# Performance work log

Measured on AMD Instinct MI355X. Metric: run time of the kernel, lower is better.

Reference implementation:

```python
import jax, jax.numpy as jnp
import numpy as np

B, C_IN, H, W = 8, 1024, 18, 80
FEAT = 1024
A = 32      # anchors per location
NCLS = 3    # classes
NREG = 13
K = 3       # kernel size
K2 = K * K
EPS = 1e-5  # BatchNorm eps


def conv2d(x, w, b):
    y = jax.lax.conv_general_dilated(x, w, (1, 1), ((1, 1), (1, 1)),
                                     dimension_numbers=('NCHW', 'OIHW', 'NCHW'))
    return y + b[None, :, None, None]


def bn_eval(x, g, b):
    # eval-mode BatchNorm2d with running_mean=0, running_var=1
    return x * (g / jnp.sqrt(1.0 + EPS))[None, :, None, None] + b[None, :, None, None]


def anchor_flatten(x, d):
    # [B, A*d, H, W] -> permute(0,2,3,1) -> [B, H*W*A, d]
    Bx, Cx, Hx, Wx = x.shape
    return jnp.transpose(x, (0, 2, 3, 1)).reshape(Bx, Hx * Wx * (Cx // d), d)


def bilinear_gather(x, py, px):
    # x: [B,C,H,W]; py/px: [B,K2,H,W] float coords -> [B,C,K2,H,W], zero outside
    Bx, Cx, Hx, Wx = x.shape
    y0 = jnp.floor(py); x0 = jnp.floor(px)
    wy1 = py - y0; wx1 = px - x0
    wy0 = 1.0 - wy1; wx0 = 1.0 - wx1
    xf = x.reshape(Bx, Cx, Hx * Wx)

    def g(yy, xx):
        valid = ((yy >= 0) & (yy < Hx) & (xx >= 0) & (xx < Wx)).astype(x.dtype)
        yc = jnp.clip(yy, 0, Hx - 1).astype(jnp.int32)
        xc = jnp.clip(xx, 0, Wx - 1).astype(jnp.int32)
        idx = (yc * Wx + xc).reshape(Bx, -1)
        vals = jax.vmap(lambda xi, ii: xi[:, ii])(xf, idx).reshape(Bx, Cx, K2, Hx, Wx)
        return vals * valid[:, None]

    return (g(y0, x0) * (wy0 * wx0)[:, None] + g(y0, x0 + 1) * (wy0 * wx1)[:, None]
            + g(y0 + 1, x0) * (wy1 * wx0)[:, None] + g(y0 + 1, x0 + 1) * (wy1 * wx1)[:, None])


def mdcn(x, off_w, off_b, w, b):
    # ModulatedDeformConvPack (DCNv2): 3x3 conv -> (dy, dx, mask), then modulated deform conv
    out = conv2d(x, off_w, off_b)                        # [B, 3*K2, H, W]
    dy, dx, m = out[:, :K2], out[:, K2:2 * K2], jax.nn.sigmoid(out[:, 2 * K2:])
    ky, kx = jnp.meshgrid(jnp.arange(K, dtype=x.dtype), jnp.arange(K, dtype=x.dtype), indexing='ij')
    base_y = jnp.arange(x.shape[2], dtype=x.dtype)[None, None, :, None] - 1.0 + ky.reshape(1, K2, 1, 1)
    base_x = jnp.arange(x.shape[3], dtype=x.dtype)[None, None, None, :] - 1.0 + kx.reshape(1, K2, 1, 1)
    sampled = bilinear_gather(x, base_y + dy, base_x + dx) * m[:, None]   # [B,C,K2,H,W]
    O = w.shape[0]
    return jnp.einsum('bckhw,ock->bohw', sampled, w.reshape(O, w.shape[1], K2)) + b[None, :, None, None]


def setup_inputs() -> dict:
    key = jax.random.key(0)
    ks = jax.random.split(key, 10)
    s1 = 1.0 / np.sqrt(C_IN * K2)
    s2 = 1.0 / np.sqrt(FEAT * K2)
    rn = lambda k, sh, sc: jax.random.normal(k, sh, jnp.float32) * sc
    return {
        'features': jax.random.normal(ks[0], (B, C_IN, H, W), jnp.float32),
        'cls_w1': rn(ks[1], (FEAT, C_IN, K, K), s1), 'cls_b1': jnp.zeros((FEAT,), jnp.float32),
        'cls_w2': rn(ks[2], (FEAT, FEAT, K, K), s2), 'cls_b2': jnp.zeros((FEAT,), jnp.float32),
        'cls_w3': rn(ks[3], (A * NCLS, FEAT, K, K), s2), 'cls_b3': jnp.zeros((A * NCLS,), jnp.float32),
        'off_w': rn(ks[4], (3 * K2, C_IN, K, K), s1), 'off_b': jnp.zeros((3 * K2,), jnp.float32),
        'dcn_w': rn(ks[5], (FEAT, C_IN, K, K), s1), 'dcn_b': jnp.zeros((FEAT,), jnp.float32),
        'bn1_g': jnp.ones((FEAT,), jnp.float32), 'bn1_b': jnp.zeros((FEAT,), jnp.float32),
        'reg_w2': rn(ks[6], (FEAT, FEAT, K, K), s2), 'reg_b2': jnp.zeros((FEAT,), jnp.float32),
        'bn2_g': jnp.ones((FEAT,), jnp.float32), 'bn2_b': jnp.zeros((FEAT,), jnp.float32),
        'reg_w3': rn(ks[7], (A * NREG, FEAT, K, K), s2), 'reg_b3': jnp.zeros((A * NREG,), jnp.float32),
    }


def reference(features, cls_w1, cls_b1, cls_w2, cls_b2, cls_w3, cls_b3,
              off_w, off_b, dcn_w, dcn_b, bn1_g, bn1_b,
              reg_w2, reg_b2, bn2_g, bn2_b, reg_w3, reg_b3):
    # cls branch (Dropout2d is identity in eval)
    h = jax.nn.relu(conv2d(features, cls_w1, cls_b1))
    h = jax.nn.relu(conv2d(h, cls_w2, cls_b2))
    cls_preds = anchor_flatten(conv2d(h, cls_w3, cls_b3), NCLS)   # [B, H*W*A, NCLS]
    # reg branch: modulated deformable conv -> BN -> ReLU -> conv -> BN -> ReLU -> conv
    r = jax.nn.relu(bn_eval(mdcn(features, off_w, off_b, dcn_w, dcn_b), bn1_g, bn1_b))
    r = jax.nn.relu(bn_eval(conv2d(r, reg_w2, reg_b2), bn2_g, bn2_b))
    reg_preds = anchor_flatten(conv2d(r, reg_w3, reg_b3), NREG)   # [B, H*W*A, NREG]
    return (cls_preds, reg_preds)
```

## Files before the change

kernel.cpp:

```cpp
#include <hip/hip_runtime.h>
#include <math.h>

typedef short short8 __attribute__((ext_vector_type(8)));
typedef float f32x4 __attribute__((ext_vector_type(4)));
typedef unsigned short u16;
typedef unsigned int u32;

#define GAS(p) ((__attribute__((address_space(1))) void*)(p))
#define LAS(p) ((__attribute__((address_space(3))) void*)(p))

namespace {

constexpr int HW   = 1440;
constexpr int PBAT = 20 * 82 * 1024;

__device__ __forceinline__ u16 f2bf(float f) {
  u32 u = __float_as_uint(f);
  return (u16)((u + 0x7FFFu + ((u >> 16) & 1u)) >> 16);
}
__device__ __forceinline__ float bf2f(u16 h) {
  return __uint_as_float(((u32)h) << 16);
}

__global__ __launch_bounds__(256)
void transpose_feat(const float* __restrict__ src, u16* __restrict__ dst) {
  __shared__ float tile[128][17];
  const int bh = blockIdx.y;
  const int b = bh / 18, h = bh % 18;
  const int wt = blockIdx.x % 5, ct = blockIdx.x / 5;
  const int w0 = wt * 16, c0 = ct * 128;
  const int tid = threadIdx.x;
#pragma unroll
  for (int it = 0; it < 8; ++it) {
    int idx = it * 256 + tid;
    int c = idx >> 4, w = idx & 15;
    tile[c][w] = src[((size_t)(b * 1024 + c0 + c) * 18 + h) * 80 + w0 + w];
  }
  __syncthreads();
  const int px = tid >> 4, cq = tid & 15;
  union { uint4 u; u16 s[8]; } pk;
#pragma unroll
  for (int j = 0; j < 8; ++j) pk.s[j] = f2bf(tile[cq * 8 + j][px]);
  *(uint4*)(dst + ((size_t)(b * 20 + h + 1) * 82 + (w0 + px + 1)) * 1024 + c0 + cq * 8) = pk.u;
}

struct RepackArgs {
  const float* src[7];
  u16* dst[7];
  int O[7];
  int start[7];
  int nseg;
};

__global__ __launch_bounds__(256)
void repack_all(RepackArgs ra) {
  int blk = blockIdx.x;
  int seg = 0;
#pragma unroll
  for (int i = 1; i < 7; ++i)
    if (i < ra.nseg && blk >= ra.start[i]) seg = i;
  const float* src = ra.src[seg];
  u16* dst = ra.dst[seg];
  const int O = ra.O[seg];
  int idx = (blk - ra.start[seg]) * 256 + threadIdx.x;
  if (idx >= O * 128) return;
  int o = idx >> 7, c8 = idx & 127;
  const float* s = src + (size_t)o * 9216 + (size_t)c8 * 72;
  float v[72];
#pragma unroll
  for (int i = 0; i < 18; ++i) {
    float4 f = *(const float4*)(s + i * 4);
    v[i * 4 + 0] = f.x; v[i * 4 + 1] = f.y; v[i * 4 + 2] = f.z; v[i * 4 + 3] = f.w;
  }
#pragma unroll
  for (int t = 0; t < 9; ++t) {
    union { uint4 u; u16 h[8]; } pk;
#pragma unroll
    for (int j = 0; j < 8; ++j) pk.h[j] = f2bf(v[j * 9 + t]);
    *(uint4*)(dst + ((size_t)t * O + o) * 1024 + c8 * 8) = pk.u;
  }
}

__device__ __forceinline__
void sample_body(int k, int lp, int pix0, int Npc,
                 const u16* __restrict__ featP, const float* __restrict__ offp,
                 u16* __restrict__ spl, int tid) {
  const int p = pix0 + lp;
  const int c8 = tid & 15;
  int b = p / HW, hw = p - b * HW;
  int h = hw / 80, w = hw - h * 80;
  float dy = offp[p * 27 + k];
  float dx = offp[p * 27 + 9 + k];
  float ml = offp[p * 27 + 18 + k];
  float m = 1.f / (1.f + expf(-ml));
  float py = (float)(h - 1 + k / 3) + dy;
  float px = (float)(w - 1 + (k % 3)) + dx;
  float y0f = floorf(py), x0f = floorf(px);
  float wy1 = py - y0f, wx1 = px - x0f;
  float wy0 = 1.f - wy1, wx0 = 1.f - wx1;
  int y0 = (int)y0f, x0 = (int)x0f;
  int ya = min(max(y0, -1), 18),  yb = min(max(y0 + 1, -1), 18);
  int xa = min(max(x0, -1), 80),  xb = min(max(x0 + 1, -1), 80);
  const u16* base = featP + (size_t)b * PBAT;
  const u16* r00 = base + ((size_t)(ya + 1) * 82 + (xa + 1)) * 1024;
  const u16* r01 = base + ((size_t)(ya + 1) * 82 + (xb + 1)) * 1024;
  const u16* r10 = base + ((size_t)(yb + 1) * 82 + (xa + 1)) * 1024;
  const u16* r11 = base + ((size_t)(yb + 1) * 82 + (xb + 1)) * 1024;
  float w00 = wy0 * wx0 * m, w01 = wy0 * wx1 * m;
  float w10 = wy1 * wx0 * m, w11 = wy1 * wx1 * m;
  u16* dst = spl + ((size_t)k * Npc + lp) * 1024;
  for (int c = c8 * 8; c < 1024; c += 128) {
    union { uint4 u; u16 h[8]; } a, bq, cq2, d, o;
    a.u   = *(const uint4*)(r00 + c);
    bq.u  = *(const uint4*)(r01 + c);
    cq2.u = *(const uint4*)(r10 + c);
    d.u   = *(const uint4*)(r11 + c);
#pragma unroll
    for (int j = 0; j < 8; ++j) {
      float v = w00 * bf2f(a.h[j]) + w01 * bf2f(bq.h[j]) +
                w10 * bf2f(cq2.h[j]) + w11 * bf2f(d.h[j]);
      o.h[j] = f2bf(v);
    }
    *(uint4*)(dst + c) = o.u;
  }
}

__global__ __launch_bounds__(256)
void sample_standalone(const u16* __restrict__ featP, const float* __restrict__ offp,
                       u16* __restrict__ spl, int pix0, int Npc) {
  sample_body(blockIdx.y, blockIdx.x * 16 + (threadIdx.x >> 4), pix0, Npc,
              featP, offp, spl, threadIdx.x);
}

struct Job {
  const u16* W; const u16* B;
  const float* bias; const float* bng; const float* bnb;
  void* out; int Co; int pix0; int Npc;
};

template<int FLAGS>
__device__ __forceinline__ void gemm_body(const Job J, int px, int oy) {
  constexpr bool PLANES  = (FLAGS & 1) != 0;
  constexpr bool F32OUT  = (FLAGS & 2) != 0;
  constexpr bool HASBN   = (FLAGS & 4) != 0;
  constexpr bool HASRELU = (FLAGS & 8) != 0;

  __shared__ __align__(16) u16 As[128 * 32];
  __shared__ __align__(16) u16 Bs[128 * 32];
  const int tid = threadIdx.x;
  const int wv = tid >> 6, lane = tid & 63;
  const int o0 = oy * 128;
  const int p0 = J.pix0 + px * 128;

  const int lr = lane >> 2;
  const int qs = (lane & 3) ^ ((lane >> 3) & 3);
  int aoff[2], boff[2];
#pragma unroll
  for (int s = 0; s < 2; ++s) {
    int r = (wv * 2 + s) * 16 + lr;
    int o = min(o0 + r, J.Co - 1);
    aoff[s] = o * 1024 + qs * 8;
    int p = p0 + r;
    if (PLANES) {
      boff[s] = (p - J.pix0) * 1024 + qs * 8;
    } else {
      int b = p / HW, hw = p - b * HW;
      int h = hw / 80, w = hw - h * 80;
      boff[s] = ((b * 20 + h) * 82 + w) * 1024 + qs * 8;
    }
  }
  u16* aDst = As + (wv * 2) * 512;
  u16* bDst = Bs + (wv * 2) * 512;

  const int wm = wv >> 1, wn = wv & 1;
  const int frm = lane & 15;
  const int kq = lane >> 4;
  const int sel = (kq ^ ((lane >> 1) & 3)) * 16;

  f32x4 acc[4][4];
#pragma unroll
  for (int i = 0; i < 4; ++i)
#pragma unroll
    for (int j = 0; j < 4; ++j) acc[i][j] = (f32x4)0.f;

  for (int t = 0; t < 9; ++t) {
    const u16* Wt = J.W + (size_t)t * J.Co * 1024;
    const u16* Bt = J.B + (PLANES ? (size_t)t * (size_t)J.Npc * 1024
                                  : (size_t)(((t / 3) * 82 + (t % 3)) * 1024));
    for (int cc = 0; cc < 1024; cc += 32) {
      __syncthreads();
#pragma unroll
      for (int s = 0; s < 2; ++s) {
        __builtin_amdgcn_global_load_lds(GAS(Wt + aoff[s] + cc), LAS(aDst + s * 512), 16, 0, 0);
        __builtin_amdgcn_global_load_lds(GAS(Bt + boff[s] + cc), LAS(bDst + s * 512), 16, 0, 0);
      }
      __syncthreads();
      uint4 af[4], bf4[4];
#pragma unroll
      for (int i = 0; i < 4; ++i) {
        af[i]  = *(const uint4*)((const char*)As + (wm * 64 + i * 16 + frm) * 64 + sel);
        bf4[i] = *(const uint4*)((const char*)Bs + (wn * 64 + i * 16 + frm) * 64 + sel);
      }
#pragma unroll
      for (int i = 0; i < 4; ++i) {
        short8 a = __builtin_bit_cast(short8, af[i]);
#pragma unroll
        for (int j = 0; j < 4; ++j) {
          short8 b = __builtin_bit_cast(short8, bf4[j]);
          acc[i][j] = __builtin_amdgcn_mfma_f32_16x16x32_bf16(a, b, acc[i][j], 0, 0, 0);
        }
      }
    }
  }

  size_t obase[4];
#pragma unroll
  for (int j = 0; j < 4; ++j) {
    int pn = p0 + wn * 64 + j * 16 + frm;
    if (F32OUT) {
      obase[j] = (size_t)pn * J.Co;
    } else {
      int b = pn / HW, hw = pn - b * HW;
      int h = hw / 80, w = hw - h * 80;
      obase[j] = ((size_t)(b * 20 + h + 1) * 82 + (w + 1)) * 1024;
    }
  }
#pragma unroll
  for (int i = 0; i < 4; ++i) {
    int o = o0 + wm * 64 + i * 16 + kq * 4;
    float bi[4], sc[4], sh[4];
#pragma unroll
    for (int r = 0; r < 4; ++r) {
      int oc = min(o + r, J.Co - 1);
      bi[r] = J.bias[oc];
      if (HASBN) { sc[r] = J.bng[oc] * rsqrtf(1.f + 1e-5f); sh[r] = J.bnb[oc]; }
    }
#pragma unroll
    for (int j = 0; j < 4; ++j) {
      float v[4];
#pragma unroll
      for (int r = 0; r < 4; ++r) {
        float x = acc[i][j][r] + bi[r];
        if (HASBN) x = x * sc[r] + sh[r];
        if (HASRELU) x = fmaxf(x, 0.f);
        v[r] = x;
      }
      if (F32OUT) {
        float* op = (float*)J.out;
#pragma unroll
        for (int r = 0; r < 4; ++r)
          if (o + r < J.Co) op[obase[j] + o + r] = v[r];
      } else {
        u16* op = (u16*)J.out;
        ushort4 pk;
        pk.x = f2bf(v[0]); pk.y = f2bf(v[1]); pk.z = f2bf(v[2]); pk.w = f2bf(v[3]);
        *(ushort4*)(op + obase[j] + o) = pk;
      }
    }
  }
}

template<int F0, int F1>
__global__ __launch_bounds__(256)
void gemm_dual(Job j0, Job j1, int ysplit) {
  int y = blockIdx.y;
  if (y < ysplit) gemm_body<F0>(j0, blockIdx.x, y);
  else            gemm_body<F1>(j1, blockIdx.x, y - ysplit);
}

template<int FLAGS>
__device__ __forceinline__ void gemm8_body(const Job J, char* ldsb, int px, int oy) {
  constexpr bool PLANES  = (FLAGS & 1) != 0;
  constexpr bool F32OUT  = (FLAGS & 2) != 0;
  constexpr bool HASBN   = (FLAGS & 4) != 0;
  constexpr bool HASRELU = (FLAGS & 8) != 0;

  const int tid = threadIdx.x;
  const int w = tid >> 6, lane = tid & 63;
  const int o0 = oy * 256;
  const int p0 = J.pix0 + px * 256;

  const int lr3 = lane >> 3;
  const int srcC = ((lane & 7) ^ lr3) << 3;
  u32 aEl[2][2], bEl[2][2];
#pragma unroll
  for (int h = 0; h < 2; ++h)
#pragma unroll
  for (int s = 0; s < 2; ++s) {
    int crow = (w * 2 + s) * 8 + lr3;
    int o = min(o0 + h * 128 + crow, J.Co - 1);
    aEl[h][s] = (u32)o * 1024u;
    int p = p0 + h * 128 + crow;
    if (PLANES) {
      bEl[h][s] = (u32)(p - J.pix0) * 1024u;
    } else {
      int b = p / HW, hw = p - b * HW;
      int hh = hw / 80, ww = hw - hh * 80;
      bEl[h][s] = (u32)((b * 20 + hh) * 82 + ww) * 1024u;
    }
  }

  auto STAGE_A = [&](int buf, int h, int kt) {
    int tap = kt >> 4, cc = (kt & 15) << 6;
    const u16* src = J.W + (size_t)tap * (size_t)J.Co * 1024 + cc + srcC;
    char* dst = ldsb + (buf * 65536 + h * 16384 + (w * 2) * 1024);
    __builtin_amdgcn_global_load_lds(GAS(src + aEl[h][0]), LAS(dst), 16, 0, 0);
    __builtin_amdgcn_global_load_lds(GAS(src + aEl[h][1]), LAS(dst + 1024), 16, 0, 0);
  };
  auto STAGE_B = [&](int buf, int h, int kt) {
    int tap = kt >> 4, cc = (kt & 15) << 6;
    size_t tb = PLANES ? (size_t)tap * (size_t)J.Npc * 1024
                       : (size_t)(((tap / 3) * 82 + (tap % 3)) * 1024);
    const u16* src = J.B + tb + cc + srcC;
    char* dst = ldsb + (buf * 65536 + 32768 + h * 16384 + (w * 2) * 1024);
    __builtin_amdgcn_global_load_lds(GAS(src + bEl[h][0]), LAS(dst), 16, 0, 0);
    __builtin_amdgcn_global_load_lds(GAS(src + bEl[h][1]), LAS(dst + 1024), 16, 0, 0);
  };

  const int wm2 = w >> 2, wn2 = w & 3;
  const int rA = wm2 * 64 + (lane & 15);
  const int rB = wn2 * 32 + (lane & 15);
  const int xsw = (lane & 7) << 4;
  const int csw0 = (((lane >> 4) << 4)) ^ xsw;
  const int csw1 = (64 | ((lane >> 4) << 4)) ^ xsw;

  f32x4 acc[4][4][2];
#pragma unroll
  for (int q = 0; q < 4; ++q)
#pragma unroll
  for (int m = 0; m < 4; ++m)
#pragma unroll
  for (int n = 0; n < 2; ++n) acc[q][m][n] = (f32x4)0.f;

  uint4 aF[4][2], bF[2][2];

#define G8_RD_A(BUF, AH)                                                      \
  { const char* Ab_ = ldsb + ((BUF) * 65536 + (AH) * 16384);                  \
    _Pragma("unroll") for (int m_ = 0; m_ < 4; ++m_) {                        \
      aF[m_][0] = *(const uint4*)(Ab_ + (rA + m_ * 16) * 128 + csw0);         \
      aF[m_][1] = *(const uint4*)(Ab_ + (rA + m_ * 16) * 128 + csw1); } }

#define G8_RD_B(BUF, BH)                                                      \
  { const char* Bb_ = ldsb + ((BUF) * 65536 + 32768 + (BH) * 16384);          \
    _Pragma("unroll") for (int n_ = 0; n_ < 2; ++n_) {                        \
      bF[n_][0] = *(const uint4*)(Bb_ + (rB + n_ * 16) * 128 + csw0);         \
      bF[n_][1] = *(const uint4*)(Bb_ + (rB + n_ * 16) * 128 + csw1); } }

#define G8_MMA(Q)                                                             \
    __builtin_amdgcn_s_barrier();                                             \
    asm volatile("s_waitcnt lgkmcnt(0)" ::: "memory");                        \
    __builtin_amdgcn_sched_barrier(0);                                        \
    __builtin_amdgcn_s_setprio(1);                                            \
    _Pragma("unroll") for (int m_ = 0; m_ < 4; ++m_)                          \
    _Pragma("unroll") for (int n_ = 0; n_ < 2; ++n_)                          \
    _Pragma("unroll") for (int k_ = 0; k_ < 2; ++k_)                          \
      acc[Q][m_][n_] = __builtin_amdgcn_mfma_f32_16x16x32_bf16(               \
          __builtin_bit_cast(short8, aF[m_][k_]),                             \
          __builtin_bit_cast(short8, bF[n_][k_]), acc[Q][m_][n_], 0, 0, 0);   \
    __builtin_amdgcn_s_setprio(0);

#define G8_VMW asm volatile("s_waitcnt vmcnt(4)" ::: "memory");
#define G8_BAR __builtin_amdgcn_s_barrier();

  STAGE_A(0, 0, 0); STAGE_A(0, 1, 0); STAGE_B(0, 0, 0); STAGE_B(0, 1, 0);
  STAGE_A(1, 0, 1); STAGE_B(1, 0, 1);
  G8_VMW
  __builtin_amdgcn_s_barrier();

  for (int it = 0; it < 72; ++it) {
    const int kt = it * 2;
    const int k2 = min(kt + 2, 143), k3 = min(kt + 3, 143);
    G8_RD_A(0, 0) G8_RD_B(0, 0) STAGE_B(1, 1, kt + 1); G8_MMA(0) G8_BAR
    G8_RD_B(0, 1)               STAGE_A(1, 1, kt + 1); G8_MMA(1) G8_BAR
    G8_RD_A(0, 1) G8_RD_B(0, 0) STAGE_A(0, 0, k2);     G8_MMA(2) G8_BAR
    G8_RD_B(0, 1)               STAGE_B(0, 0, k2);     G8_MMA(3) G8_VMW G8_BAR
    G8_RD_A(1, 0) G8_RD_B(1, 0) STAGE_B(0, 1, k2);     G8_MMA(0) G8_BAR
    G8_RD_B(1, 1)               STAGE_A(0, 1, k2);     G8_MMA(1) G8_BAR
    G8_RD_A(1, 1) G8_RD_B(1, 0) STAGE_A(1, 0, k3);     G8_MMA(2) G8_BAR
    G8_RD_B(1, 1)               STAGE_B(1, 0, k3);     G8_MMA(3) G8_VMW G8_BAR
  }

#undef G8_RD_A
#undef G8_RD_B
#undef G8_MMA
#undef G8_VMW
#undef G8_BAR

  const int kq = lane >> 4, fr = lane & 15;
  size_t pixB[2][2];
#pragma unroll
  for (int bh = 0; bh < 2; ++bh)
#pragma unroll
  for (int n = 0; n < 2; ++n) {
    int p = p0 + bh * 128 + wn2 * 32 + n * 16 + fr;
    if (F32OUT) {
      pixB[bh][n] = (size_t)p * J.Co;
    } else {
      int b = p / HW, hw = p - b * HW;
      int hh = hw / 80, ww = hw - hh * 80;
      pixB[bh][n] = ((size_t)(b * 20 + hh + 1) * 82 + (ww + 1)) * 1024;
    }
  }
#pragma unroll
  for (int ah = 0; ah < 2; ++ah)
#pragma unroll
  for (int m = 0; m < 4; ++m) {
    int ob = o0 + ah * 128 + wm2 * 64 + m * 16 + kq * 4;
    float bi[4], sc[4], sh[4];
#pragma unroll
    for (int r = 0; r < 4; ++r) {
      int oc = min(ob + r, J.Co - 1);
      bi[r] = J.bias[oc];
      if (HASBN) { sc[r] = J.bng[oc] * rsqrtf(1.f + 1e-5f); sh[r] = J.bnb[oc]; }
    }
#pragma unroll
    for (int bh = 0; bh < 2; ++bh)
#pragma unroll
    for (int n = 0; n < 2; ++n) {
      float v[4];
#pragma unroll
      for (int r = 0; r < 4; ++r) {
        float x = acc[ah * 2 + bh][m][n][r] + bi[r];
        if (HASBN) x = x * sc[r] + sh[r];
        if (HASRELU) x = fmaxf(x, 0.f);
        v[r] = x;
      }
      if (F32OUT) {
        float* op = (float*)J.out;
#pragma unroll
        for (int r = 0; r < 4; ++r)
          if (ob + r < J.Co) op[pixB[bh][n] + ob + r] = v[r];
      } else {
        u16* op = (u16*)J.out;
        ushort4 pk;
        pk.x = f2bf(v[0]); pk.y = f2bf(v[1]); pk.z = f2bf(v[2]); pk.w = f2bf(v[3]);
        *(ushort4*)(op + pixB[bh][n] + ob) = pk;
      }
    }
  }
}

template<int F0, int F1>
__global__ __launch_bounds__(512, 2)
void gemm8_dual(Job j0, Job j1, int n0, int mt0, int mt1) {
  __shared__ __align__(16) char ldsb[131072];
  int x = blockIdx.x;
  if (x < n0) gemm8_body<F0>(j0, ldsb, x / mt0, x % mt0);
  else { x -= n0; gemm8_body<F1>(j1, ldsb, x / mt1, x % mt1); }
}

template<int F0>
__global__ __launch_bounds__(512, 2)
void gemm8_sample(Job j, const u16* __restrict__ featP, const float* __restrict__ offp,
                  u16* __restrict__ spl, int n0, int mt0) {
  __shared__ __align__(16) char ldsb[131072];
  int x = blockIdx.x;
  if (x < n0) {
    gemm8_body<F0>(j, ldsb, x / mt0, x % mt0);
  } else {
    int sidx = x - n0;
    int k = sidx / 360, bs = sidx % 360;
    sample_body(k, bs * 32 + ((int)threadIdx.x >> 4), 0, 11520,
                featP, offp, spl, (int)threadIdx.x);
  }
}

}

extern "C" void kernel_launch(void* const* d_in, const int* in_sizes, int n_in,
                              void* d_out, int out_size, void* d_ws, size_t ws_size,
                              hipStream_t stream) {
  const float* feat   = (const float*)d_in[0];
  const float* cls_w1 = (const float*)d_in[1];
  const float* cls_b1 = (const float*)d_in[2];
  const float* cls_w2 = (const float*)d_in[3];
  const float* cls_b2 = (const float*)d_in[4];
  const float* cls_w3 = (const float*)d_in[5];
  const float* cls_b3 = (const float*)d_in[6];
  const float* off_w  = (const float*)d_in[7];
  const float* off_b  = (const float*)d_in[8];
  const float* dcn_w  = (const float*)d_in[9];
  const float* dcn_b  = (const float*)d_in[10];
  const float* bn1_g  = (const float*)d_in[11];
  const float* bn1_b  = (const float*)d_in[12];
  const float* reg_w2 = (const float*)d_in[13];
  const float* reg_b2 = (const float*)d_in[14];
  const float* bn2_g  = (const float*)d_in[15];
  const float* bn2_b  = (const float*)d_in[16];
  const float* reg_w3 = (const float*)d_in[17];
  const float* reg_b3 = (const float*)d_in[18];
  float* outp = (float*)d_out;

  const size_t ACTB = 26869760;
  char* wsb = (char*)d_ws;
  u16* featP = (u16*)(wsb);
  u16* bufA  = (u16*)(wsb + ACTB);
  u16* bufB  = (u16*)(wsb + 2 * ACTB);
  u16* wts   = (u16*)(wsb + 3 * ACTB);
  float* offp = (float*)(wsb + 3 * ACTB + 85432320);
  u16* spl   = (u16*)(wsb + 3 * ACTB + 85432320 + 1244160);
  const size_t BASE = 3 * ACTB + 85432320 + 1244160;
  const size_t SPLB = (size_t)9 * 11520 * 1024 * 2;

  u16* offT = wts;
  u16* w1T  = wts + 248832;
  u16* w2T  = wts + 9686016;
  u16* w3T  = wts + 19123200;
  u16* dcnT = wts + 20007936;
  u16* r2T  = wts + 29445120;
  u16* r3T  = wts + 38882304;

  dim3 blk(256);

  hipMemsetAsync(featP, 0, 3 * ACTB, stream);
  transpose_feat<<<dim3(40, 144), blk, 0, stream>>>(feat, featP);

  {
    RepackArgs ra;
    const float* s[7] = {off_w, cls_w1, cls_w2, cls_w3, dcn_w, reg_w2, reg_w3};
    u16* d[7] = {offT, w1T, w2T, w3T, dcnT, r2T, r3T};
    int  O[7] = {27, 1024, 1024, 96, 1024, 1024, 416};
    int acc = 0;
    for (int i = 0; i < 7; ++i) {
      ra.src[i] = s[i]; ra.dst[i] = d[i]; ra.O[i] = O[i]; ra.start[i] = acc;
      acc += (O[i] * 128 + 255) / 256;
    }
    ra.nseg = 7;
    repack_all<<<dim3(acc), blk, 0, stream>>>(ra);
  }

  Job jOff  = {offT, featP, off_b, nullptr, nullptr, offp, 27, 0, 0};
  Job jCls1 = {w1T, featP, cls_b1, nullptr, nullptr, bufA, 1024, 0, 0};
  Job jCls2 = {w2T, bufA, cls_b2, nullptr, nullptr, bufB, 1024, 0, 0};
  Job jCls3 = {w3T, bufB, cls_b3, nullptr, nullptr, outp, 96, 0, 0};
  Job jReg2 = {r2T, bufA, reg_b2, bn2_g, bn2_b, bufB, 1024, 0, 0};
  Job jReg3 = {r3T, bufB, reg_b3, nullptr, nullptr, outp + 1105920, 416, 0, 0};

  if (ws_size >= BASE + SPLB) {
    dim3 b512(512);
    gemm8_dual<8, 2><<<dim3(225), b512, 0, stream>>>(jCls1, jOff, 180, 4, 1);
    gemm8_sample<8><<<dim3(180 + 3240), b512, 0, stream>>>(jCls2, featP, offp, spl, 180, 4);
    Job jDcn = {dcnT, spl, dcn_b, bn1_g, bn1_b, bufA, 1024, 0, 11520};
    gemm8_dual<1 | 4 | 8, 2><<<dim3(225), b512, 0, stream>>>(jDcn, jCls3, 180, 4, 1);
    gemm8_dual<4 | 8, 4 | 8><<<dim3(180), b512, 0, stream>>>(jReg2, jReg2, 180, 4, 4);
    gemm_dual<2, 2><<<dim3(90, 4), blk, 0, stream>>>(jReg3, jReg3, 4);
  } else {
    gemm_dual<8, 2><<<dim3(90, 9), blk, 0, stream>>>(jCls1, jOff, 8);
    gemm_dual<8, 8><<<dim3(90, 8), blk, 0, stream>>>(jCls2, jCls2, 8);
    size_t avail = ws_size > BASE ? ws_size - BASE : 0;
    int tiles = (int)(avail / 2359296);
    if (tiles < 1) tiles = 1;
    if (tiles > 90) tiles = 90;
    for (int t0 = 0; t0 < 90; t0 += tiles) {
      int nt = (90 - t0) < tiles ? (90 - t0) : tiles;
      int pix0 = t0 * 128, np = nt * 128;
      sample_standalone<<<dim3(nt * 8, 9), blk, 0, stream>>>(featP, offp, spl, pix0, np);
      Job jDcn = {dcnT, spl, dcn_b, bn1_g, bn1_b, bufA, 1024, pix0, np};
      gemm_dual<1 | 4 | 8, 1 | 4 | 8><<<dim3(nt, 8), blk, 0, stream>>>(jDcn, jDcn, 8);
    }
    gemm_dual<2, 2><<<dim3(90, 1), blk, 0, stream>>>(jCls3, jCls3, 1);
    gemm_dual<4 | 8, 4 | 8><<<dim3(90, 8), blk, 0, stream>>>(jReg2, jReg2, 8);
    gemm_dual<2, 2><<<dim3(90, 4), blk, 0, stream>>>(jReg3, jReg3, 4);
  }
}
```

Measured before the change: 2.161 ms.

## Add double-buffered chunked DCN path overlapping sampling with DCN GEMM

Adds a middle path for workspaces too small for the full sampled buffer. DCN pixels are split into chunks held in two ping-pong sample buffers, and each launch fuses the DCN GEMM for the current chunk with sampling for the next chunk. The first launch also carries the cls3 GEMM. This replaces the serial sample-then-GEMM tile loop and its extra launches, at the cost of using the smaller 256-thread GEMM body for DCN and more launches than the full-buffer path.

```diff
diff --git a/kernel.cpp b/kernel.cpp
--- a/kernel.cpp
+++ b/kernel.cpp
@@ -268,6 +268,22 @@
   else            gemm_body<F1>(j1, blockIdx.x, y - ysplit);
 }
 
+template<int F0, int F1>
+__global__ __launch_bounds__(256)
+void dcn_chunk(Job j0, Job j1, int n0, int nt0, int n1,
+               const u16* __restrict__ featP, const float* __restrict__ offp,
+               u16* __restrict__ splNext, int pix0n, int npn) {
+  int x = blockIdx.x;
+  if (x < n0) { gemm_body<F0>(j0, x % nt0, x / nt0); return; }
+  x -= n0;
+  if (x < n1) { gemm_body<F1>(j1, x % 90, x / 90); return; }
+  x -= n1;
+  int per = npn >> 4;
+  int k = x / per, bs = x % per;
+  sample_body(k, bs * 16 + ((int)threadIdx.x >> 4), pix0n, npn,
+              featP, offp, splNext, (int)threadIdx.x);
+}
+
 template<int FLAGS>
 __device__ __forceinline__ void gemm8_body(const Job J, char* ldsb, int px, int oy) {
   constexpr bool PLANES  = (FLAGS & 1) != 0;
@@ -452,15 +468,16 @@
 template<int F0>
 __global__ __launch_bounds__(512, 2)
 void gemm8_sample(Job j, const u16* __restrict__ featP, const float* __restrict__ offp,
-                  u16* __restrict__ spl, int n0, int mt0) {
+                  u16* __restrict__ spl, int n0, int mt0, int pix0s, int nps) {
   __shared__ __align__(16) char ldsb[131072];
   int x = blockIdx.x;
   if (x < n0) {
     gemm8_body<F0>(j, ldsb, x / mt0, x % mt0);
   } else {
     int sidx = x - n0;
-    int k = sidx / 360, bs = sidx % 360;
-    sample_body(k, bs * 32 + ((int)threadIdx.x >> 4), 0, 11520,
+    int per = nps >> 5;
+    int k = sidx / per, bs = sidx % per;
+    sample_body(k, bs * 32 + ((int)threadIdx.x >> 4), pix0s, nps,
                 featP, offp, spl, (int)threadIdx.x);
   }
 }
@@ -511,6 +528,7 @@
   u16* r3T  = wts + 38882304;
 
   dim3 blk(256);
+  dim3 b512(512);
 
   hipMemsetAsync(featP, 0, 3 * ACTB, stream);
   transpose_feat<<<dim3(40, 144), blk, 0, stream>>>(feat, featP);
@@ -536,26 +554,56 @@
   Job jReg2 = {r2T, bufA, reg_b2, bn2_g, bn2_b, bufB, 1024, 0, 0};
   Job jReg3 = {r3T, bufB, reg_b3, nullptr, nullptr, outp + 1105920, 416, 0, 0};
 
-  if (ws_size >= BASE + SPLB) {
-    dim3 b512(512);
+  size_t avail = ws_size > BASE ? ws_size - BASE : 0;
+
+  int tch = 0;
+  {
+    const int cand[5] = {30, 18, 15, 10, 9};
+    for (int i = 0; i < 5; ++i)
+      if ((size_t)2 * cand[i] * 2359296 <= avail) { tch = cand[i]; break; }
+  }
+
+  if (avail >= SPLB) {
     gemm8_dual<8, 2><<<dim3(225), b512, 0, stream>>>(jCls1, jOff, 180, 4, 1);
-    gemm8_sample<8><<<dim3(180 + 3240), b512, 0, stream>>>(jCls2, featP, offp, spl, 180, 4);
+    gemm8_sample<8><<<dim3(180 + 3240), b512, 0, stream>>>(jCls2, featP, offp, spl, 180, 4, 0, 11520);
     Job jDcn = {dcnT, spl, dcn_b, bn1_g, bn1_b, bufA, 1024, 0, 11520};
     gemm8_dual<1 | 4 | 8, 2><<<dim3(225), b512, 0, stream>>>(jDcn, jCls3, 180, 4, 1);
+    gemm8_dual<4 | 8, 4 | 8><<<dim3(180), b512, 0, stream>>>(jReg2, jReg2, 180, 4, 4);
+    gemm_dual<2, 2><<<dim3(90, 4), blk, 0, stream>>>(jReg3, jReg3, 4);
+  } else if (tch > 0) {
+    const int C = 90 / tch;
+    const int np = tch * 128;
+    u16* splA = spl;
+    u16* splB = spl + (size_t)tch * 1179648;
+
+    gemm8_dual<8, 2><<<dim3(225), b512, 0, stream>>>(jCls1, jOff, 180, 4, 1);
+    gemm8_sample<8><<<dim3(180 + 9 * (np / 32)), b512, 0, stream>>>(
+        jCls2, featP, offp, splA, 180, 4, 0, np);
+    for (int i = 0; i < C; ++i) {
+      u16* sCur  = (i & 1) ? splB : splA;
+      u16* sNext = (i & 1) ? splA : splB;
+      Job jDcnC = {dcnT, sCur, dcn_b, bn1_g, bn1_b, bufA, 1024, i * np, np};
+      int n0 = tch * 8;
+      int n1 = (i == 0) ? 90 : 0;
+      bool hasS = (i + 1 < C);
+      int ns = hasS ? 9 * (np / 16) : 0;
+      dcn_chunk<1 | 4 | 8, 2><<<dim3(n0 + n1 + ns), blk, 0, stream>>>(
+          jDcnC, jCls3, n0, tch, n1,
+          featP, offp, sNext, (i + 1) * np, hasS ? np : 16);
+    }
     gemm8_dual<4 | 8, 4 | 8><<<dim3(180), b512, 0, stream>>>(jReg2, jReg2, 180, 4, 4);
     gemm_dual<2, 2><<<dim3(90, 4), blk, 0, stream>>>(jReg3, jReg3, 4);
   } else {
     gemm_dual<8, 2><<<dim3(90, 9), blk, 0, stream>>>(jCls1, jOff, 8);
     gemm_dual<8, 8><<<dim3(90, 8), blk, 0, stream>>>(jCls2, jCls2, 8);
-    size_t avail = ws_size > BASE ? ws_size - BASE : 0;
     int tiles = (int)(avail / 2359296);
     if (tiles < 1) tiles = 1;
     if (tiles > 90) tiles = 90;
     for (int t0 = 0; t0 < 90; t0 += tiles) {
       int nt = (90 - t0) < tiles ? (90 - t0) : tiles;
-      int pix0 = t0 * 128, np = nt * 128;
-      sample_standalone<<<dim3(nt * 8, 9), blk, 0, stream>>>(featP, offp, spl, pix0, np);
-      Job jDcn = {dcnT, spl, dcn_b, bn1_g, bn1_b, bufA, 1024, pix0, np};
+      int pix0 = t0 * 128, npp = nt * 128;
+      sample_standalone<<<dim3(nt * 8, 9), blk, 0, stream>>>(featP, offp, spl, pix0, npp);
+      Job jDcn = {dcnT, spl, dcn_b, bn1_g, bn1_b, bufA, 1024, pix0, npp};
       gemm_dual<1 | 4 | 8, 1 | 4 | 8><<<dim3(nt, 8), blk, 0, stream>>>(jDcn, jDcn, 8);
     }
     gemm_dual<2, 2><<<dim3(90, 1), blk, 0, stream>>>(jCls3, jCls3, 1);
```

New measurement: 2.622 ms. 1.21x slower.
